# Kernel optimization log

Measured on AMD Instinct MI355X. Metric: run time of the kernel, lower is better.

## Reference

```python
import jax, jax.numpy as jnp
import numpy as np

ROPE_BASE = 10000.0
NEG_INF = -1e30

def _apply_rope(x):
    # x: [B, H, T, D]; interleaved-pair RoPE (torchtune style), positions along axis -2.
    B, H, T, D = x.shape
    inv_freq = 1.0 / (ROPE_BASE ** (jnp.arange(0, D, 2, dtype=jnp.float32) / D))  # [D/2]
    ang = jnp.arange(T, dtype=jnp.float32)[:, None] * inv_freq[None, :]           # [T, D/2]
    cos, sin = jnp.cos(ang), jnp.sin(ang)
    x1, x2 = x[..., 0::2], x[..., 1::2]                                           # [B,H,T,D/2]
    rot = jnp.stack([x1 * cos - x2 * sin, x1 * sin + x2 * cos], axis=-1)          # [B,H,T,D/2,2]
    return rot.reshape(B, H, T, D).astype(x.dtype)

def setup_inputs() -> dict:
    key = jax.random.key(0)
    ks = jax.random.split(key, 5)
    B, T, C = 2, 2048, 1024
    s = 1.0 / np.sqrt(C)
    return {
        "x":  jax.random.normal(ks[0], (B, T, C), jnp.float32),
        "Wq": jax.random.normal(ks[1], (C, C), jnp.float32) * s,
        "bq": jnp.zeros((C,), jnp.float32),
        "Wk": jax.random.normal(ks[2], (C, C), jnp.float32) * s,
        "bk": jnp.zeros((C,), jnp.float32),
        "Wv": jax.random.normal(ks[3], (C, C), jnp.float32) * s,
        "bv": jnp.zeros((C,), jnp.float32),
        "Wo": jax.random.normal(ks[4], (C, C), jnp.float32) * s,
        "bo": jnp.zeros((C,), jnp.float32),
    }

def reference(x, Wq, bq, Wk, bk, Wv, bv, Wo, bo):
    B, T, C = x.shape
    H = 16
    D = C // H
    # QKV projections (torch Linear: x @ W.T + b), split heads -> [B, H, T, D]
    def proj(W, b):
        return (jnp.einsum('btc,oc->bto', x, W) + b).reshape(B, T, H, D).transpose(0, 2, 1, 3)
    q = _apply_rope(proj(Wq, bq))
    k = _apply_rope(proj(Wk, bk))
    v = proj(Wv, bv)
    # Causal scaled dot-product attention
    scale = 1.0 / jnp.sqrt(jnp.asarray(D, x.dtype))
    scores = jnp.einsum('bhqd,bhkd->bhqk', q, k) * scale                          # [B,H,T,T]
    causal = jnp.tril(jnp.ones((T, T), dtype=bool))
    scores = jnp.where(causal, scores, NEG_INF)
    probs = jax.nn.softmax(scores, axis=-1)
    y = jnp.einsum('bhqk,bhkd->bhqd', probs, v)                                   # [B,H,T,D]
    y = y.transpose(0, 2, 1, 3).reshape(B, T, C)
    # Output projection (dropout is identity in eval mode)
    return jnp.einsum('btc,oc->bto', y, Wo) + bo
```

## Files before the change

kernel.cpp:

```cpp
#include <hip/hip_runtime.h>

#define BB 2
#define TT 2048
#define CC 1024
#define HH 16
#define DD 64
#define KDIM 1024
#define MROWS (BB*TT)

typedef __attribute__((ext_vector_type(8))) short  frag_b16;
typedef __attribute__((ext_vector_type(4))) float  f32x4;
typedef __attribute__((ext_vector_type(4))) unsigned short us4;
typedef __attribute__((ext_vector_type(8))) unsigned short us8;
typedef __attribute__((ext_vector_type(4))) _Float16 f16x4;
typedef __attribute__((ext_vector_type(8))) _Float16 f16x8;

#define EXP2F(x) __builtin_amdgcn_exp2f(x)

__device__ __forceinline__ unsigned short f2bf(float f) {
    unsigned int u = __builtin_bit_cast(unsigned int, f);
    u += 0x7FFFu + ((u >> 16) & 1u);
    return (unsigned short)(u >> 16);
}

__device__ __forceinline__ void gl_lds16(const void* g, void* l) {
    __builtin_amdgcn_global_load_lds(
        (const __attribute__((address_space(1))) unsigned int*)g,
        (__attribute__((address_space(3))) unsigned int*)l, 16, 0, 0);
}

__global__ __launch_bounds__(256) void cvt_all(
        const float* __restrict__ x,  const float* __restrict__ w0,
        const float* __restrict__ w1, const float* __restrict__ w2,
        const float* __restrict__ w3, unsigned short* __restrict__ dst) {
    const size_t NX = (size_t)MROWS * CC;
    const size_t NW = (size_t)CC * CC;
    size_t i = ((size_t)blockIdx.x * 256 + threadIdx.x) * 4;
    const float* src; size_t off;
    if (i < NX) { src = x; off = i; }
    else {
        size_t j = i - NX;
        int t = (int)(j >> 20);
        src = (t == 0) ? w0 : (t == 1) ? w1 : (t == 2) ? w2 : w3;
        off = j & (NW - 1);
    }
    float4 f = *reinterpret_cast<const float4*>(src + off);
    us4 o;
    o.x = f2bf(f.x); o.y = f2bf(f.y); o.z = f2bf(f.z); o.w = f2bf(f.w);
    *reinterpret_cast<us4*>(dst + i) = o;
}

__global__ __launch_bounds__(256, 2) void qkv_gemm_rope(
        const unsigned short* __restrict__ X,
        const unsigned short* __restrict__ Wq,
        const unsigned short* __restrict__ Wk,
        const unsigned short* __restrict__ Wv,
        const float* __restrict__ bq, const float* __restrict__ bk,
        const float* __restrict__ bv,
        unsigned short* __restrict__ Qo,
        unsigned short* __restrict__ Ko,
        _Float16* __restrict__ VTo)
{
    const int z = blockIdx.z;
    const unsigned short* W = (z == 0) ? Wq : (z == 1) ? Wk : Wv;
    const float* bias = (z == 0) ? bq : (z == 1) ? bk : bv;

    const int tid = threadIdx.x;
    const int wave = tid >> 6;
    const int lane = tid & 63;
    const int l16 = lane & 15;
    const int quad = lane >> 4;

    const int bx = blockIdx.x * 128;
    const int by = blockIdx.y * 128;
    const int row0 = bx + (wave >> 1) * 64;
    const int col0 = by + (wave & 1) * 64;

    __shared__ __align__(16) char smem[36864];
    unsigned short* Xa0 = (unsigned short*)smem;
    unsigned short* Wb0 = (unsigned short*)(smem + 16384);
    _Float16 (*Vl)[64][72] = (_Float16(*)[64][72])smem;

    f32x4 acc[4][4] = {};

    int srow[4]; int scol[4];
#pragma unroll
    for (int i = 0; i < 4; ++i) {
        int n = tid + 256 * i;
        srow[i] = n >> 3;
        scol[i] = ((n & 7) ^ (srow[i] & 7)) * 8;
    }

    const int ar = (wave >> 1) * 64;
    const int bc = (wave & 1) * 64;

#pragma unroll 1
    for (int step = 0; step < 16; ++step) {
        __syncthreads();
        const int kk = step * 64;
#pragma unroll
        for (int i = 0; i < 4; ++i) {
            int n = tid + 256 * i;
            gl_lds16(X + (size_t)(bx + srow[i]) * KDIM + kk + scol[i], Xa0 + n * 8);
            gl_lds16(W + (size_t)(by + srow[i]) * KDIM + kk + scol[i], Wb0 + n * 8);
        }
        asm volatile("s_waitcnt vmcnt(0)" ::: "memory");
        __syncthreads();

        frag_b16 a[4][2], b[4][2];
#pragma unroll
        for (int r = 0; r < 4; ++r) {
            int row = ar + r * 16 + l16;
#pragma unroll
            for (int kh = 0; kh < 2; ++kh) {
                int c = (kh * 4 + quad) ^ (row & 7);
                a[r][kh] = *reinterpret_cast<const frag_b16*>(
                    Xa0 + row * 64 + c * 8);
            }
        }
#pragma unroll
        for (int cc = 0; cc < 4; ++cc) {
            int row = bc + cc * 16 + l16;
#pragma unroll
            for (int kh = 0; kh < 2; ++kh) {
                int c = (kh * 4 + quad) ^ (row & 7);
                b[cc][kh] = *reinterpret_cast<const frag_b16*>(
                    Wb0 + row * 64 + c * 8);
            }
        }
#pragma unroll
        for (int r = 0; r < 4; ++r)
#pragma unroll
            for (int c = 0; c < 4; ++c) {
                acc[r][c] = __builtin_amdgcn_mfma_f32_16x16x32_bf16(a[r][0], b[c][0], acc[r][c], 0, 0, 0);
                acc[r][c] = __builtin_amdgcn_mfma_f32_16x16x32_bf16(a[r][1], b[c][1], acc[r][c], 0, 0, 0);
            }
    }

    __syncthreads();

    if (z == 2) {
#pragma unroll
        for (int r = 0; r < 4; ++r)
#pragma unroll
            for (int c = 0; c < 4; ++c) {
                f16x4 pk;
#pragma unroll
                for (int g = 0; g < 4; ++g)
                    pk[g] = (_Float16)(acc[r][c][g] + bias[col0 + c * 16 + l16]);
                *reinterpret_cast<f16x4*>(&Vl[wave][c * 16 + l16][r * 16 + quad * 4]) = pk;
            }
        const int b_ = row0 >> 11;
        const int t_base = row0 & (TT - 1);
        const int h = col0 >> 6;
        const int dl = lane >> 3;
        const int t8 = (lane & 7) * 8;
        __builtin_amdgcn_s_waitcnt(0);
#pragma unroll
        for (int i = 0; i < 8; ++i) {
            int d = i * 8 + dl;
            f16x8 v = *reinterpret_cast<const f16x8*>(&Vl[wave][d][t8]);
            *reinterpret_cast<f16x8*>(
                &VTo[((size_t)(b_ * HH + h) * DD + d) * TT + t_base + t8]) = v;
        }
    } else {
        const float qsc = (z == 0) ? 0.180336888f : 1.0f;
        unsigned short* dst = (z == 0) ? Qo : Ko;
        const int b_ = row0 >> 11;
        const int tq0 = (row0 & (TT - 1)) + quad * 4;
#pragma unroll
        for (int c = 0; c < 4; ++c) {
            const int o = col0 + c * 16 + l16;
            const int h = o >> 6, d = o & (DD - 1);
            const float inv = __expf(-(float)(d & ~1) * (9.210340371976184f / (float)DD));
            float cs0, sn0, cs1, sn1, cs16, sn16;
            __sincosf((float)tq0 * inv, &sn0, &cs0);
            __sincosf(inv, &sn1, &cs1);
            __sincosf(16.f * inv, &sn16, &cs16);
            float cr = cs0, sr = sn0;
#pragma unroll
            for (int r = 0; r < 4; ++r) {
                float cg = cr, sg = sr;
#pragma unroll
                for (int g = 0; g < 4; ++g) {
                    int n = row0 + r * 16 + quad * 4 + g;
                    int t = n & (TT - 1);
                    float v = acc[r][c][g] + bias[o];
                    float pv = __shfl_xor(v, 1);
                    float outv = (d & 1) ? (pv * sg + v * cg) : (v * cg - pv * sg);
                    dst[((size_t)(b_ * HH + h) * TT + t) * DD + d] = f2bf(outv * qsc);
                    float cn = cg * cs1 - sg * sn1;
                    sg = sg * cs1 + cg * sn1;
                    cg = cn;
                }
                float crn = cr * cs16 - sr * sn16;
                sr = sr * cs16 + cr * sn16;
                cr = crn;
            }
        }
    }
}

__global__ __launch_bounds__(256, 2) void attn(
        const unsigned short* __restrict__ Q,
        const unsigned short* __restrict__ K,
        const _Float16* __restrict__ VT,
        unsigned short* __restrict__ Y)
{
    const int b1d = blockIdx.x;
    const int bh = (b1d & 7) * 4 + ((b1d >> 3) & 3);
    const int pair = b1d >> 5;
    const int tid = threadIdx.x;
    const int w = tid >> 6;
    const int lane = tid & 63;
    const int l16 = lane & 15;
    const int quad = lane >> 4;

    const unsigned short* Qp = Q + (size_t)bh * TT * DD;
    const unsigned short* Kp = K + (size_t)bh * TT * DD;
    const _Float16* Vp = VT + (size_t)bh * DD * TT;

    __shared__ unsigned short Kl[2][128][64];
    __shared__ _Float16 Vl[2][64][128];
    __shared__ unsigned short Ylds[4][16][72];

    const int sw = (l16 & 7);
    const int b_ = bh >> 4, h = bh & (HH - 1);

    f16x8 ones8;
#pragma unroll
    for (int j = 0; j < 8; ++j) ones8[j] = (_Float16)1.0f;

#pragma unroll 1
    for (int seg = 0; seg < 2; ++seg) {
        const int qblk = seg ? (31 - pair) : pair;
        const int q0 = qblk * 64;
        const int q = q0 + w * 16 + l16;

        frag_b16 bq[2];
#pragma unroll
        for (int dk = 0; dk < 2; ++dk)
            bq[dk] = *reinterpret_cast<const frag_b16*>(
                Qp + (size_t)q * DD + dk * 32 + quad * 8);

        f32x4 yacc[4] = {};
        f32x4 lsum = {};

        const int ntiles = (qblk >> 1) + 1;

#pragma unroll
        for (int i = 0; i < 4; ++i) {
            int n = tid + 256 * i;
            int kr = n >> 3,  kc = ((n & 7)  ^ ((kr & 3) | ((kr >> 1) & 4))) * 8;
            int vr = n >> 4,  vc = ((n & 15) ^ (vr & 7)) * 8;
            gl_lds16(Kp + (size_t)kr * DD + kc, (unsigned short*)&Kl[0][0][0] + n * 8);
            gl_lds16(Vp + (size_t)vr * TT + vc, (_Float16*)&Vl[0][0][0] + n * 8);
        }

#pragma unroll 1
        for (int it = 0; it < ntiles; ++it) {
            __syncthreads();
            const int bsel = it & 1;
            if (it + 1 < ntiles) {
                const int jn = (it + 1) * 128;
                const int bn = bsel ^ 1;
#pragma unroll
                for (int i = 0; i < 4; ++i) {
                    int n = tid + 256 * i;
                    int kr = n >> 3,  kc = ((n & 7)  ^ ((kr & 3) | ((kr >> 1) & 4))) * 8;
                    int vr = n >> 4,  vc = ((n & 15) ^ (vr & 7)) * 8;
                    gl_lds16(Kp + (size_t)(jn + kr) * DD + kc,
                             (unsigned short*)&Kl[bn][0][0] + n * 8);
                    gl_lds16(Vp + (size_t)vr * TT + jn + vc,
                             (_Float16*)&Vl[bn][0][0] + n * 8);
                }
            }
            const int j0 = it * 128;

            f32x4 s[8];
            const int swr = l16 & 7;
#pragma unroll
            for (int mt = 0; mt < 8; ++mt) {
                const int r = (mt >> 1) * 32 + ((l16 >> 2) * 8) + (mt & 1) * 4 + (l16 & 3);
                frag_b16 ak0 = *reinterpret_cast<const frag_b16*>(
                    &Kl[bsel][r][(quad ^ swr) * 8]);
                frag_b16 ak1 = *reinterpret_cast<const frag_b16*>(
                    &Kl[bsel][r][((4 + quad) ^ swr) * 8]);
                f32x4 t = {};
                t = __builtin_amdgcn_mfma_f32_16x16x32_bf16(ak0, bq[0], t, 0, 0, 0);
                t = __builtin_amdgcn_mfma_f32_16x16x32_bf16(ak1, bq[1], t, 0, 0, 0);
                s[mt] = t;
            }

            if (it == ntiles - 1) {
#pragma unroll
                for (int mt = 0; mt < 8; ++mt)
#pragma unroll
                    for (int g = 0; g < 4; ++g) {
                        int key = j0 + (mt >> 1) * 32 + quad * 8 + (mt & 1) * 4 + g;
                        if (key > q) s[mt][g] = -1e30f;
                    }
            }

            f16x8 pw[4];
#pragma unroll
            for (int w32 = 0; w32 < 4; ++w32)
#pragma unroll
                for (int g = 0; g < 4; ++g) {
                    pw[w32][g]     = (_Float16)EXP2F(s[2 * w32][g]     - 11.0f);
                    pw[w32][g + 4] = (_Float16)EXP2F(s[2 * w32 + 1][g] - 11.0f);
                }

#pragma unroll
            for (int w32 = 0; w32 < 4; ++w32)
                lsum = __builtin_amdgcn_mfma_f32_16x16x32_f16(ones8, pw[w32], lsum, 0, 0, 0);

#pragma unroll
            for (int dt = 0; dt < 4; ++dt) {
                f32x4 ya = yacc[dt];
#pragma unroll
                for (int w32 = 0; w32 < 4; ++w32) {
                    f16x8 av = *reinterpret_cast<const f16x8*>(
                        &Vl[bsel][dt * 16 + l16][((w32 * 4 + quad) ^ sw) * 8]);
                    ya = __builtin_amdgcn_mfma_f32_16x16x32_f16(av, pw[w32], ya, 0, 0, 0);
                }
                yacc[dt] = ya;
            }
        }

        __syncthreads();

        float rl = 1.f / lsum[0];
#pragma unroll
        for (int dt = 0; dt < 4; ++dt)
#pragma unroll
            for (int g = 0; g < 4; ++g)
                Ylds[w][l16][dt * 16 + quad * 4 + g] = f2bf(yacc[dt][g] * rl);

#pragma unroll
        for (int i = 0; i < 2; ++i) {
            int idx = i * 64 + lane;
            int r = idx >> 3, c8 = (idx & 7) * 8;
            us8 v = *reinterpret_cast<const us8*>(&Ylds[w][r][c8]);
            *reinterpret_cast<us8*>(
                &Y[(size_t)(b_ * TT + q0 + w * 16 + r) * CC + h * DD + c8]) = v;
        }
    }
}

__global__ __launch_bounds__(256, 2) void out_gemm(
        const unsigned short* __restrict__ Y,
        const unsigned short* __restrict__ Wo,
        const float* __restrict__ bo,
        float* __restrict__ out)
{
    const int tid = threadIdx.x;
    const int wave = tid >> 6;
    const int lane = tid & 63;
    const int l16 = lane & 15;
    const int quad = lane >> 4;

    const int bx = blockIdx.x * 128;
    const int by = blockIdx.y * 128;
    const int row0 = bx + (wave >> 1) * 64;
    const int col0 = by + (wave & 1) * 64;

    __shared__ __align__(16) char smem[65536];
    unsigned short* Xa0 = (unsigned short*)smem;
    unsigned short* Wb0 = (unsigned short*)(smem + 32768);

    f32x4 acc[4][4] = {};

    int srow[4]; int scol[4];
#pragma unroll
    for (int i = 0; i < 4; ++i) {
        int n = tid + 256 * i;
        srow[i] = n >> 3;
        scol[i] = ((n & 7) ^ (srow[i] & 7)) * 8;
    }

#pragma unroll
    for (int i = 0; i < 4; ++i) {
        int n = tid + 256 * i;
        gl_lds16(Y  + (size_t)(bx + srow[i]) * KDIM + scol[i], Xa0 + n * 8);
        gl_lds16(Wo + (size_t)(by + srow[i]) * KDIM + scol[i], Wb0 + n * 8);
    }

    const int ar = (wave >> 1) * 64;
    const int bc = (wave & 1) * 64;

#pragma unroll 1
    for (int step = 0; step < 16; ++step) {
        __syncthreads();
        const int bsel = step & 1;
        if (step + 1 < 16) {
            const int kk = (step + 1) * 64;
            const int bo_ = (bsel ^ 1) * 8192;
#pragma unroll
            for (int i = 0; i < 4; ++i) {
                int n = tid + 256 * i;
                gl_lds16(Y  + (size_t)(bx + srow[i]) * KDIM + kk + scol[i],
                         Xa0 + bo_ + n * 8);
                gl_lds16(Wo + (size_t)(by + srow[i]) * KDIM + kk + scol[i],
                         Wb0 + bo_ + n * 8);
            }
        }

        frag_b16 a[4][2], b[4][2];
#pragma unroll
        for (int r = 0; r < 4; ++r) {
            int row = ar + r * 16 + l16;
#pragma unroll
            for (int kh = 0; kh < 2; ++kh) {
                int c = (kh * 4 + quad) ^ (row & 7);
                a[r][kh] = *reinterpret_cast<const frag_b16*>(
                    Xa0 + bsel * 8192 + row * 64 + c * 8);
            }
        }
#pragma unroll
        for (int cc = 0; cc < 4; ++cc) {
            int row = bc + cc * 16 + l16;
#pragma unroll
            for (int kh = 0; kh < 2; ++kh) {
                int c = (kh * 4 + quad) ^ (row & 7);
                b[cc][kh] = *reinterpret_cast<const frag_b16*>(
                    Wb0 + bsel * 8192 + row * 64 + c * 8);
            }
        }
#pragma unroll
        for (int r = 0; r < 4; ++r)
#pragma unroll
            for (int c = 0; c < 4; ++c) {
                acc[r][c] = __builtin_amdgcn_mfma_f32_16x16x32_bf16(a[r][0], b[c][0], acc[r][c], 0, 0, 0);
                acc[r][c] = __builtin_amdgcn_mfma_f32_16x16x32_bf16(a[r][1], b[c][1], acc[r][c], 0, 0, 0);
            }
    }

#pragma unroll
    for (int r = 0; r < 4; ++r)
#pragma unroll
        for (int c = 0; c < 4; ++c)
#pragma unroll
            for (int g = 0; g < 4; ++g) {
                int n = row0 + r * 16 + quad * 4 + g;
                int o = col0 + c * 16 + l16;
                out[(size_t)n * CC + o] = acc[r][c][g] + bo[o];
            }
}

extern "C" void kernel_launch(void* const* d_in, const int* in_sizes, int n_in,
                              void* d_out, int out_size, void* d_ws, size_t ws_size,
                              hipStream_t stream) {
    const float* x  = (const float*)d_in[0];
    const float* Wq = (const float*)d_in[1];
    const float* bq = (const float*)d_in[2];
    const float* Wk = (const float*)d_in[3];
    const float* bk = (const float*)d_in[4];
    const float* Wv = (const float*)d_in[5];
    const float* bv = (const float*)d_in[6];
    const float* Wo = (const float*)d_in[7];
    const float* bo = (const float*)d_in[8];
    float* out = (float*)d_out;

    unsigned short* ws = (unsigned short*)d_ws;
    const size_t NX = (size_t)MROWS * CC;
    const size_t NW = (size_t)CC * CC;
    unsigned short* xb  = ws;
    unsigned short* wqb = xb  + NX;
    unsigned short* wkb = wqb + NW;
    unsigned short* wvb = wkb + NW;
    unsigned short* wob = wvb + NW;
    unsigned short* Qr  = wob + NW;
    unsigned short* Kr  = Qr  + NX;
    _Float16*       VTb = (_Float16*)(Kr + NX);
    unsigned short* Yb  = (unsigned short*)(VTb + NX);

    const size_t NALL = NX + 4 * NW;
    cvt_all<<<dim3((unsigned)(NALL / 1024)), 256, 0, stream>>>(x, Wq, Wk, Wv, Wo, xb);

    qkv_gemm_rope<<<dim3(MROWS / 128, CC / 128, 3), 256, 0, stream>>>(
        xb, wqb, wkb, wvb, bq, bk, bv, Qr, Kr, VTb);

    attn<<<dim3(512), 256, 0, stream>>>(Qr, Kr, VTb, Yb);

    out_gemm<<<dim3(MROWS / 128, CC / 128), 256, 0, stream>>>(Yb, wob, bo, out);
}
```

Baseline: 161.1 us.

## Split attention into one query block per workgroup, drop K/V double buffering

The attention kernel now launches one workgroup per 64-row query block, ordered heaviest first (qblk = 31 - index), instead of pairing a light and a heavy block in one workgroup. It also replaces the double-buffered K/V LDS staging with a single buffer that is loaded, waited on and synchronised each tile. This halves LDS use and doubles the grid, aiming for more occupancy and better load balance. In exchange it loses the overlap of the global-to-LDS copy with the MFMA work.

```diff
diff --git a/kernel.cpp b/kernel.cpp
--- a/kernel.cpp
+++ b/kernel.cpp
@@ -209,7 +209,7 @@
 {
     const int b1d = blockIdx.x;
     const int bh = (b1d & 7) * 4 + ((b1d >> 3) & 3);
-    const int pair = b1d >> 5;
+    const int qblk = 31 - (b1d >> 5);
     const int tid = threadIdx.x;
     const int w = tid >> 6;
     const int lane = tid & 63;
@@ -220,8 +220,8 @@
     const unsigned short* Kp = K + (size_t)bh * TT * DD;
     const _Float16* Vp = VT + (size_t)bh * DD * TT;
 
-    __shared__ unsigned short Kl[2][128][64];
-    __shared__ _Float16 Vl[2][64][128];
+    __shared__ unsigned short Kl[128][64];
+    __shared__ _Float16 Vl[64][128];
     __shared__ unsigned short Ylds[4][16][72];
 
     const int sw = (l16 & 7);
@@ -231,120 +231,102 @@
 #pragma unroll
     for (int j = 0; j < 8; ++j) ones8[j] = (_Float16)1.0f;
 
+    const int q0 = qblk * 64;
+    const int q = q0 + w * 16 + l16;
+
+    frag_b16 bq[2];
+#pragma unroll
+    for (int dk = 0; dk < 2; ++dk)
+        bq[dk] = *reinterpret_cast<const frag_b16*>(
+            Qp + (size_t)q * DD + dk * 32 + quad * 8);
+
+    f32x4 yacc[4] = {};
+    f32x4 lsum = {};
+
+    const int ntiles = (qblk >> 1) + 1;
+
 #pragma unroll 1
-    for (int seg = 0; seg < 2; ++seg) {
-        const int qblk = seg ? (31 - pair) : pair;
-        const int q0 = qblk * 64;
-        const int q = q0 + w * 16 + l16;
-
-        frag_b16 bq[2];
-#pragma unroll
-        for (int dk = 0; dk < 2; ++dk)
-            bq[dk] = *reinterpret_cast<const frag_b16*>(
-                Qp + (size_t)q * DD + dk * 32 + quad * 8);
-
-        f32x4 yacc[4] = {};
-        f32x4 lsum = {};
-
-        const int ntiles = (qblk >> 1) + 1;
-
+    for (int it = 0; it < ntiles; ++it) {
+        __syncthreads();
+        const int j0 = it * 128;
 #pragma unroll
         for (int i = 0; i < 4; ++i) {
             int n = tid + 256 * i;
             int kr = n >> 3,  kc = ((n & 7)  ^ ((kr & 3) | ((kr >> 1) & 4))) * 8;
             int vr = n >> 4,  vc = ((n & 15) ^ (vr & 7)) * 8;
-            gl_lds16(Kp + (size_t)kr * DD + kc, (unsigned short*)&Kl[0][0][0] + n * 8);
-            gl_lds16(Vp + (size_t)vr * TT + vc, (_Float16*)&Vl[0][0][0] + n * 8);
-        }
-
-#pragma unroll 1
-        for (int it = 0; it < ntiles; ++it) {
-            __syncthreads();
-            const int bsel = it & 1;
-            if (it + 1 < ntiles) {
-                const int jn = (it + 1) * 128;
-                const int bn = bsel ^ 1;
-#pragma unroll
-                for (int i = 0; i < 4; ++i) {
-                    int n = tid + 256 * i;
-                    int kr = n >> 3,  kc = ((n & 7)  ^ ((kr & 3) | ((kr >> 1) & 4))) * 8;
-                    int vr = n >> 4,  vc = ((n & 15) ^ (vr & 7)) * 8;
-                    gl_lds16(Kp + (size_t)(jn + kr) * DD + kc,
-                             (unsigned short*)&Kl[bn][0][0] + n * 8);
-                    gl_lds16(Vp + (size_t)vr * TT + jn + vc,
-                             (_Float16*)&Vl[bn][0][0] + n * 8);
+            gl_lds16(Kp + (size_t)(j0 + kr) * DD + kc,
+                     (unsigned short*)&Kl[0][0] + n * 8);
+            gl_lds16(Vp + (size_t)vr * TT + j0 + vc,
+                     (_Float16*)&Vl[0][0] + n * 8);
+        }
+        asm volatile("s_waitcnt vmcnt(0)" ::: "memory");
+        __syncthreads();
+
+        f32x4 s[8];
+        const int swr = l16 & 7;
+#pragma unroll
+        for (int mt = 0; mt < 8; ++mt) {
+            const int r = (mt >> 1) * 32 + ((l16 >> 2) * 8) + (mt & 1) * 4 + (l16 & 3);
+            frag_b16 ak0 = *reinterpret_cast<const frag_b16*>(
+                &Kl[r][(quad ^ swr) * 8]);
+            frag_b16 ak1 = *reinterpret_cast<const frag_b16*>(
+                &Kl[r][((4 + quad) ^ swr) * 8]);
+            f32x4 t = {};
+            t = __builtin_amdgcn_mfma_f32_16x16x32_bf16(ak0, bq[0], t, 0, 0, 0);
+            t = __builtin_amdgcn_mfma_f32_16x16x32_bf16(ak1, bq[1], t, 0, 0, 0);
+            s[mt] = t;
+        }
+
+        if (it == ntiles - 1) {
+#pragma unroll
+            for (int mt = 0; mt < 8; ++mt)
+#pragma unroll
+                for (int g = 0; g < 4; ++g) {
+                    int key = j0 + (mt >> 1) * 32 + quad * 8 + (mt & 1) * 4 + g;
+                    if (key > q) s[mt][g] = -1e30f;
                 }
-            }
-            const int j0 = it * 128;
-
-            f32x4 s[8];
-            const int swr = l16 & 7;
-#pragma unroll
-            for (int mt = 0; mt < 8; ++mt) {
-                const int r = (mt >> 1) * 32 + ((l16 >> 2) * 8) + (mt & 1) * 4 + (l16 & 3);
-                frag_b16 ak0 = *reinterpret_cast<const frag_b16*>(
-                    &Kl[bsel][r][(quad ^ swr) * 8]);
-                frag_b16 ak1 = *reinterpret_cast<const frag_b16*>(
-                    &Kl[bsel][r][((4 + quad) ^ swr) * 8]);
-                f32x4 t = {};
-                t = __builtin_amdgcn_mfma_f32_16x16x32_bf16(ak0, bq[0], t, 0, 0, 0);
-                t = __builtin_amdgcn_mfma_f32_16x16x32_bf16(ak1, bq[1], t, 0, 0, 0);
-                s[mt] = t;
-            }
-
-            if (it == ntiles - 1) {
-#pragma unroll
-                for (int mt = 0; mt < 8; ++mt)
-#pragma unroll
-                    for (int g = 0; g < 4; ++g) {
-                        int key = j0 + (mt >> 1) * 32 + quad * 8 + (mt & 1) * 4 + g;
-                        if (key > q) s[mt][g] = -1e30f;
-                    }
-            }
-
-            f16x8 pw[4];
-#pragma unroll
-            for (int w32 = 0; w32 < 4; ++w32)
-#pragma unroll
-                for (int g = 0; g < 4; ++g) {
-                    pw[w32][g]     = (_Float16)EXP2F(s[2 * w32][g]     - 11.0f);
-                    pw[w32][g + 4] = (_Float16)EXP2F(s[2 * w32 + 1][g] - 11.0f);
-                }
-
-#pragma unroll
-            for (int w32 = 0; w32 < 4; ++w32)
-                lsum = __builtin_amdgcn_mfma_f32_16x16x32_f16(ones8, pw[w32], lsum, 0, 0, 0);
-
-#pragma unroll
-            for (int dt = 0; dt < 4; ++dt) {
-                f32x4 ya = yacc[dt];
-#pragma unroll
-                for (int w32 = 0; w32 < 4; ++w32) {
-                    f16x8 av = *reinterpret_cast<const f16x8*>(
-                        &Vl[bsel][dt * 16 + l16][((w32 * 4 + quad) ^ sw) * 8]);
-                    ya = __builtin_amdgcn_mfma_f32_16x16x32_f16(av, pw[w32], ya, 0, 0, 0);
-                }
-                yacc[dt] = ya;
-            }
-        }
-
-        __syncthreads();
-
-        float rl = 1.f / lsum[0];
-#pragma unroll
-        for (int dt = 0; dt < 4; ++dt)
-#pragma unroll
-            for (int g = 0; g < 4; ++g)
-                Ylds[w][l16][dt * 16 + quad * 4 + g] = f2bf(yacc[dt][g] * rl);
-
-#pragma unroll
-        for (int i = 0; i < 2; ++i) {
-            int idx = i * 64 + lane;
-            int r = idx >> 3, c8 = (idx & 7) * 8;
-            us8 v = *reinterpret_cast<const us8*>(&Ylds[w][r][c8]);
-            *reinterpret_cast<us8*>(
-                &Y[(size_t)(b_ * TT + q0 + w * 16 + r) * CC + h * DD + c8]) = v;
-        }
+        }
+
+        f16x8 pw[4];
+#pragma unroll
+        for (int w32 = 0; w32 < 4; ++w32)
+#pragma unroll
+            for (int g = 0; g < 4; ++g) {
+                pw[w32][g]     = (_Float16)EXP2F(s[2 * w32][g]     - 11.0f);
+                pw[w32][g + 4] = (_Float16)EXP2F(s[2 * w32 + 1][g] - 11.0f);
+            }
+
+#pragma unroll
+        for (int w32 = 0; w32 < 4; ++w32)
+            lsum = __builtin_amdgcn_mfma_f32_16x16x32_f16(ones8, pw[w32], lsum, 0, 0, 0);
+
+#pragma unroll
+        for (int dt = 0; dt < 4; ++dt) {
+            f32x4 ya = yacc[dt];
+#pragma unroll
+            for (int w32 = 0; w32 < 4; ++w32) {
+                f16x8 av = *reinterpret_cast<const f16x8*>(
+                    &Vl[dt * 16 + l16][((w32 * 4 + quad) ^ sw) * 8]);
+                ya = __builtin_amdgcn_mfma_f32_16x16x32_f16(av, pw[w32], ya, 0, 0, 0);
+            }
+            yacc[dt] = ya;
+        }
+    }
+
+    float rl = 1.f / lsum[0];
+#pragma unroll
+    for (int dt = 0; dt < 4; ++dt)
+#pragma unroll
+        for (int g = 0; g < 4; ++g)
+            Ylds[w][l16][dt * 16 + quad * 4 + g] = f2bf(yacc[dt][g] * rl);
+
+#pragma unroll
+    for (int i = 0; i < 2; ++i) {
+        int idx = i * 64 + lane;
+        int r = idx >> 3, c8 = (idx & 7) * 8;
+        us8 v = *reinterpret_cast<const us8*>(&Ylds[w][r][c8]);
+        *reinterpret_cast<us8*>(
+            &Y[(size_t)(b_ * TT + q0 + w * 16 + r) * CC + h * DD + c8]) = v;
     }
 }
 
@@ -481,7 +463,7 @@
     qkv_gemm_rope<<<dim3(MROWS / 128, CC / 128, 3), 256, 0, stream>>>(
         xb, wqb, wkb, wvb, bq, bk, bv, Qr, Kr, VTb);
 
-    attn<<<dim3(512), 256, 0, stream>>>(Qr, Kr, VTb, Yb);
+    attn<<<dim3(1024), 256, 0, stream>>>(Qr, Kr, VTb, Yb);
 
     out_gemm<<<dim3(MROWS / 128, CC / 128), 256, 0, stream>>>(Yb, wob, bo, out);
 }
```

After: 161.7 us. No clear change (+0.3%).
